# Kernel optimization log

Hardware: AMD Instinct MI355X
Metric: run time of the kernel (lower is better)

Reference implementation:

```python
import jax, jax.numpy as jnp
import numpy as np

B, A, M, C = 8, 100000, 32, 80
ALPHA, GAMMA = 0.25, 2.0
NORM = np.array([[0.1, 0.1, 0.2, 0.2]], dtype=np.float32)


def setup_inputs() -> dict:
    key = jax.random.key(0)
    k1, k2, k3, k4, k5, k6, k7, k8 = jax.random.split(key, 8)
    classifications = jax.random.uniform(k1, (B, A, C), dtype=jnp.float32)
    reggressions = jax.random.normal(k2, (B, A, 4), dtype=jnp.float32)
    # valid anchors: positive width/height boxes inside a ~640px image
    ctr = jax.random.uniform(k3, (1, A, 2), dtype=jnp.float32) * 600.0 + 20.0
    wh = jax.random.uniform(k4, (1, A, 2), dtype=jnp.float32) * 96.0 + 16.0
    anchors = jnp.concatenate([ctr - 0.5 * wh, ctr + 0.5 * wh], axis=-1)
    # annotations: [x1,y1,x2,y2,class], class=-1 marks padding
    xy1 = jax.random.uniform(k5, (B, M, 2), dtype=jnp.float32) * 500.0
    gwh = jax.random.uniform(k6, (B, M, 2), dtype=jnp.float32) * 112.0 + 8.0
    cls = jax.random.randint(k7, (B, M), 0, C).astype(jnp.float32)
    pad = jax.random.uniform(k8, (B, M)) < 0.3
    cls = jnp.where(pad, -1.0, cls)
    annotations = jnp.concatenate([xy1, xy1 + gwh, cls[..., None]], axis=-1)
    return {"classifications": classifications, "reggressions": reggressions,
            "anchors": anchors, "annotations": annotations}


def _calc_iou(a, b):
    # a: [A,4], b: [M,4] -> [A,M]
    area = (b[:, 2] - b[:, 0]) * (b[:, 3] - b[:, 1])
    iw = jnp.minimum(a[:, 2, None], b[None, :, 2]) - jnp.maximum(a[:, 0, None], b[None, :, 0])
    ih = jnp.minimum(a[:, 3, None], b[None, :, 3]) - jnp.maximum(a[:, 1, None], b[None, :, 1])
    iw = jnp.clip(iw, 0.0)
    ih = jnp.clip(ih, 0.0)
    ua = ((a[:, 2] - a[:, 0]) * (a[:, 3] - a[:, 1]))[:, None] + area[None, :] - iw * ih
    ua = jnp.clip(ua, 1e-8)
    return iw * ih / ua


def _focal_loss(classifications, reggressions, anchors, annotations):
    anchor = anchors[0]  # [A,4]
    aw = anchor[:, 2] - anchor[:, 0]
    ah = anchor[:, 3] - anchor[:, 1]
    acx = anchor[:, 0] + 0.5 * aw
    acy = anchor[:, 1] + 0.5 * ah
    norm = jnp.asarray(NORM)

    def per_image(cls_p, reg_p, annot):
        valid = annot[:, 4] != -1.0  # [M]
        has_valid = valid.any()
        cls_p = jnp.clip(cls_p, 1e-4, 1.0 - 1e-4)
        iou = _calc_iou(anchor, annot[:, :4])            # [A,M]
        iou = jnp.where(valid[None, :], iou, -1.0)       # mask padded annots
        iou_max = iou.max(axis=1)                        # [A]
        iou_arg = iou.argmax(axis=1)                     # [A]
        assigned = annot[iou_arg]                        # [A,5]
        pos = iou_max >= 0.5
        neg = iou_max < 0.4
        onehot = jax.nn.one_hot(assigned[:, 4].astype(jnp.int32), cls_p.shape[-1], dtype=cls_p.dtype)
        targets = jnp.where(pos[:, None], onehot,
                            jnp.where(neg[:, None], 0.0, -1.0))  # [A,C]
        alpha_f = jnp.where(targets == 1.0, ALPHA, 1.0 - ALPHA)
        focal_w = jnp.where(targets == 1.0, 1.0 - cls_p, cls_p)
        focal_w = alpha_f * focal_w ** GAMMA
        bce = -(targets * jnp.log(cls_p) + (1.0 - targets) * jnp.log(1.0 - cls_p))
        cls_loss = jnp.where(targets != -1.0, focal_w * bce, 0.0)
        num_pos = pos.sum().astype(cls_p.dtype)
        cls_total = jnp.where(has_valid,
                              cls_loss.sum() / jnp.maximum(num_pos, 1.0), 0.0)
        gw = jnp.clip(assigned[:, 2] - assigned[:, 0], 0.0)
        gh = jnp.clip(assigned[:, 3] - assigned[:, 1], 0.0)
        gcx = assigned[:, 0] + 0.5 * (assigned[:, 2] - assigned[:, 0])
        gcy = assigned[:, 1] + 0.5 * (assigned[:, 3] - assigned[:, 1])
        dx = (gcx - acx) / aw
        dy = (gcy - acy) / ah
        dw = jnp.log(jnp.where(pos, gw, aw) / aw)  # safe log on non-positives
        dh = jnp.log(jnp.where(pos, gh, ah) / ah)
        t = jnp.stack([dx, dy, dw, dh], axis=1) / norm  # [A,4]
        diff = jnp.abs(t - reg_p)
        rl = jnp.where(diff <= 1.0 / 9.0, 0.5 * 9.0 * diff ** 2, diff - 5.0 / 9.0)
        reg_total = jnp.where(num_pos > 0,
                              (rl * pos[:, None]).sum() / (4.0 * jnp.maximum(num_pos, 1.0)),
                              0.0)
        return cls_total, reg_total

    cls_l, reg_l = jax.vmap(per_image)(classifications, reggressions, annotations)
    return cls_l.mean().reshape(1), reg_l.mean().reshape(1)


def reference(classifications, reggressions, anchors, annotations):
    return _focal_loss(classifications, reggressions, anchors, annotations)
```

## Files before the change

kernel.cpp:

```cpp
#include <hip/hip_runtime.h>
#include <cstdint>
#include <cstddef>

#define NB 8
#define NA 100000
#define NM 32
#define NC 80
#define BLK 256
#define NBLK ((NA + BLK - 1) / BLK)
#define LN2F 0.69314718056f


__global__ __launch_bounds__(256) void fused_kernel(
    const float* __restrict__ cls,
    const float* __restrict__ regs,
    const float* __restrict__ anchors,
    const float* __restrict__ annots,
    float4* __restrict__ parts)
{
    const int b   = blockIdx.y;
    const int blk = blockIdx.x;
    const int tid = threadIdx.x;
    const int a   = blk * BLK + tid;

    __shared__ float sann[NM * 5];
    __shared__ float sw[BLK];
    __shared__ float sred[4 * 3];

    if (tid < NM * 5) sann[tid] = annots[b * NM * 5 + tid];
    __syncthreads();

    float reg_acc = 0.f;
    float posf    = 0.f;
    float corr    = 0.f;
    int   st      = 201;

    if (a < NA) {
        const float4 av = reinterpret_cast<const float4*>(anchors)[a];
        const float ax1 = av.x, ay1 = av.y, ax2 = av.z, ay2 = av.w;
        const float aw = ax2 - ax1, ah = ay2 - ay1;
        const float aarea = aw * ah;

        float best = -1e30f;
        int   barg = 0;
        #pragma unroll
        for (int m = 0; m < NM; ++m) {
            const float bx1 = sann[m * 5 + 0];
            const float by1 = sann[m * 5 + 1];
            const float bx2 = sann[m * 5 + 2];
            const float by2 = sann[m * 5 + 3];
            const float bc  = sann[m * 5 + 4];
            const float area = (bx2 - bx1) * (by2 - by1);
            float iw = fminf(ax2, bx2) - fmaxf(ax1, bx1);
            float ih = fminf(ay2, by2) - fmaxf(ay1, by1);
            iw = fmaxf(iw, 0.f);
            ih = fmaxf(ih, 0.f);
            const float inter = iw * ih;
            const float ua = fmaxf(aarea + area - inter, 1e-8f);
            float iou = inter * __builtin_amdgcn_rcpf(ua);
            if (bc == -1.0f) iou = -1.0f;
            if (iou > best) { best = iou; barg = m; }
        }

        if (best >= 0.5f) {
            const float bx1 = sann[barg * 5 + 0];
            const float by1 = sann[barg * 5 + 1];
            const float bx2 = sann[barg * 5 + 2];
            const float by2 = sann[barg * 5 + 3];
            st   = (int)sann[barg * 5 + 4];
            posf = 1.f;
            const float gw  = fmaxf(bx2 - bx1, 0.f);
            const float gh  = fmaxf(by2 - by1, 0.f);
            const float gcx = bx1 + 0.5f * (bx2 - bx1);
            const float gcy = by1 + 0.5f * (by2 - by1);
            const float acx = ax1 + 0.5f * aw;
            const float acy = ay1 + 0.5f * ah;
            const float t0 = ((gcx - acx) / aw) * 10.f;
            const float t1 = ((gcy - acy) / ah) * 10.f;
            const float t2 = __logf(gw / aw) * 5.f;
            const float t3 = __logf(gh / ah) * 5.f;
            const float4 rp = reinterpret_cast<const float4*>(regs)[(size_t)b * NA + a];
            const float d0 = fabsf(t0 - rp.x);
            const float d1 = fabsf(t1 - rp.y);
            const float d2 = fabsf(t2 - rp.z);
            const float d3 = fabsf(t3 - rp.w);
            const float TH = 1.f / 9.f;
            const float C59 = 5.f / 9.f;
            reg_acc  = (d0 <= TH) ? 4.5f * d0 * d0 : d0 - C59;
            reg_acc += (d1 <= TH) ? 4.5f * d1 * d1 : d1 - C59;
            reg_acc += (d2 <= TH) ? 4.5f * d2 * d2 : d2 - C59;
            reg_acc += (d3 <= TH) ? 4.5f * d3 * d3 : d3 - C59;
            const float pr  = cls[((size_t)b * NA + a) * NC + st];
            const float pt  = __builtin_amdgcn_fmed3f(pr, 1e-4f, 0.9999f);
            const float omt = 1.f - pt;
            corr = -0.25f * omt * omt * __logf(pt) + 0.75f * (pt * pt) * __logf(omt);
        } else if (best < 0.4f) {
            st = 200;
        }
    }
    sw[tid] = (st == 201) ? 0.f : 0.75f;
    __syncthreads();

    const int na_blk = min(BLK, NA - blk * BLK);
    const int n4 = na_blk * (NC / 4);
    const float4* __restrict__ p4 =
        reinterpret_cast<const float4*>(cls) + ((size_t)b * NA + (size_t)blk * BLK) * (NC / 4);

    float sneg = 0.f;
    int al  = tid / 20;
    int rem = tid - al * 20;
    #pragma unroll 5
    for (int k = 0; k < BLK * (NC / 4) / BLK; ++k) {
        const int i   = k * BLK + tid;
        const int ild = min(i, n4 - 1);
        const float4 v = p4[ild];
        const float wgt = (i < n4) ? sw[al] : 0.f;
        float g = 0.f;
        {
            const float p0 = __builtin_amdgcn_fmed3f(v.x, 1e-4f, 0.9999f);
            g = __fmaf_rn(p0 * p0, __log2f(1.f - p0), g);
            const float p1 = __builtin_amdgcn_fmed3f(v.y, 1e-4f, 0.9999f);
            g = __fmaf_rn(p1 * p1, __log2f(1.f - p1), g);
            const float p2 = __builtin_amdgcn_fmed3f(v.z, 1e-4f, 0.9999f);
            g = __fmaf_rn(p2 * p2, __log2f(1.f - p2), g);
            const float p3 = __builtin_amdgcn_fmed3f(v.w, 1e-4f, 0.9999f);
            g = __fmaf_rn(p3 * p3, __log2f(1.f - p3), g);
        }
        sneg = __fmaf_rn(wgt, g, sneg);
        rem += 16;
        const int c = (rem >= 20) ? 1 : 0;
        al  += 12 + c;
        rem -= c * 20;
    }

    float cacc = __fmaf_rn(-LN2F, sneg, corr);

    float r = reg_acc;
    float p = posf;
    #pragma unroll
    for (int off = 32; off; off >>= 1) {
        cacc += __shfl_down(cacc, off);
        r    += __shfl_down(r, off);
        p    += __shfl_down(p, off);
    }
    const int w = tid >> 6;
    if ((tid & 63) == 0) {
        sred[w * 3 + 0] = cacc;
        sred[w * 3 + 1] = r;
        sred[w * 3 + 2] = p;
    }
    __syncthreads();
    if (tid == 0) {
        float C = 0.f, R = 0.f, P = 0.f;
        #pragma unroll
        for (int i = 0; i < 4; ++i) {
            C += sred[i * 3 + 0];
            R += sred[i * 3 + 1];
            P += sred[i * 3 + 2];
        }
        parts[b * NBLK + blk] = make_float4(C, R, P, 0.f);
    }
}

__global__ __launch_bounds__(512) void finalize_kernel(
    const float* __restrict__ annots,
    const float4* __restrict__ parts,
    float* __restrict__ out)
{
    const int tid  = threadIdx.x;
    const int b    = tid >> 6;
    const int lane = tid & 63;
    __shared__ float simg[NB * 2];

    float C = 0.f, R = 0.f, P = 0.f;
    for (int i = lane; i < NBLK; i += 64) {
        const float4 v = parts[b * NBLK + i];
        C += v.x; R += v.y; P += v.z;
    }
    #pragma unroll
    for (int off = 32; off; off >>= 1) {
        C += __shfl_down(C, off);
        R += __shfl_down(R, off);
        P += __shfl_down(P, off);
    }
    const bool vld = (lane < NM) && (annots[b * NM * 5 + lane * 5 + 4] != -1.0f);
    const unsigned long long m = __ballot(vld);
    if (lane == 0) {
        const bool hv = (m != 0ULL);
        const float d = fmaxf(P, 1.f);
        simg[b * 2 + 0] = hv ? C / d : 0.f;
        simg[b * 2 + 1] = (P > 0.f) ? R / (4.f * d) : 0.f;
    }
    __syncthreads();
    if (tid == 0) {
        float cm = 0.f, rm = 0.f;
        #pragma unroll
        for (int i = 0; i < NB; ++i) {
            cm += simg[i * 2 + 0];
            rm += simg[i * 2 + 1];
        }
        out[0] = cm * (1.f / NB);
        out[1] = rm * (1.f / NB);
    }
}

extern "C" void kernel_launch(void* const* d_in, const int* in_sizes, int n_in,
                              void* d_out, int out_size, void* d_ws, size_t ws_size,
                              hipStream_t stream) {
    const float* cls     = (const float*)d_in[0];
    const float* regs    = (const float*)d_in[1];
    const float* anchors = (const float*)d_in[2];
    const float* annots  = (const float*)d_in[3];
    float* out = (float*)d_out;

    float4* parts = (float4*)d_ws;

    dim3 g1(NBLK, NB);
    fused_kernel<<<g1, BLK, 0, stream>>>(cls, regs, anchors, annots, parts);
    finalize_kernel<<<1, 512, 0, stream>>>(annots, parts, out);
}
```

Baseline: 50.30 us.

## Prefetch classification tiles before IoU phase and double-buffer the negative-loss stream

Block size grows from 256 to 512 threads, with the anchor-to-class index stepping constants and the reduction buffer resized to match. The first four float4 classification loads, plus the anchor load, are issued before the initial barrier so they overlap the IoU/argmax phase. The negative focal-loss loop is restructured into five groups of four loads, with the next group prefetched while the current one is computed. This aims to hide global memory latency in a bandwidth-bound stream, at the cost of more registers per thread and fewer blocks per CU.

```diff
diff --git a/kernel.cpp b/kernel.cpp
--- a/kernel.cpp
+++ b/kernel.cpp
@@ -6,12 +6,27 @@
 #define NA 100000
 #define NM 32
 #define NC 80
-#define BLK 256
+#define BLK 512
 #define NBLK ((NA + BLK - 1) / BLK)
 #define LN2F 0.69314718056f
 
-
-__global__ __launch_bounds__(256) void fused_kernel(
+#define ALQ 25
+#define ALR 12
+
+
+__device__ __forceinline__ float neg_term(const float4 v) {
+    const float p0 = __builtin_amdgcn_fmed3f(v.x, 1e-4f, 0.9999f);
+    float g = p0 * p0 * __log2f(1.f - p0);
+    const float p1 = __builtin_amdgcn_fmed3f(v.y, 1e-4f, 0.9999f);
+    g = __fmaf_rn(p1 * p1, __log2f(1.f - p1), g);
+    const float p2 = __builtin_amdgcn_fmed3f(v.z, 1e-4f, 0.9999f);
+    g = __fmaf_rn(p2 * p2, __log2f(1.f - p2), g);
+    const float p3 = __builtin_amdgcn_fmed3f(v.w, 1e-4f, 0.9999f);
+    g = __fmaf_rn(p3 * p3, __log2f(1.f - p3), g);
+    return g;
+}
+
+__global__ __launch_bounds__(512) void fused_kernel(
     const float* __restrict__ cls,
     const float* __restrict__ regs,
     const float* __restrict__ anchors,
@@ -25,9 +40,23 @@
 
     __shared__ float sann[NM * 5];
     __shared__ float sw[BLK];
-    __shared__ float sred[4 * 3];
+    __shared__ float sred[8 * 3];
 
     if (tid < NM * 5) sann[tid] = annots[b * NM * 5 + tid];
+
+    const float4 av = reinterpret_cast<const float4*>(anchors)[min(a, NA - 1)];
+
+    const int na_blk = min(BLK, NA - blk * BLK);
+    const int n4     = na_blk * (NC / 4);
+    const int n4m1   = n4 - 1;
+    const float4* __restrict__ p4 =
+        reinterpret_cast<const float4*>(cls) + ((size_t)b * NA + (size_t)blk * BLK) * (NC / 4);
+
+    float4 v0 = p4[min(0 * BLK + tid, n4m1)];
+    float4 v1 = p4[min(1 * BLK + tid, n4m1)];
+    float4 v2 = p4[min(2 * BLK + tid, n4m1)];
+    float4 v3 = p4[min(3 * BLK + tid, n4m1)];
+
     __syncthreads();
 
     float reg_acc = 0.f;
@@ -36,7 +65,6 @@
     int   st      = 201;
 
     if (a < NA) {
-        const float4 av = reinterpret_cast<const float4*>(anchors)[a];
         const float ax1 = av.x, ay1 = av.y, ax2 = av.z, ay2 = av.w;
         const float aw = ax2 - ax1, ah = ay2 - ay1;
         const float aarea = aw * ah;
@@ -101,36 +129,34 @@
     sw[tid] = (st == 201) ? 0.f : 0.75f;
     __syncthreads();
 
-    const int na_blk = min(BLK, NA - blk * BLK);
-    const int n4 = na_blk * (NC / 4);
-    const float4* __restrict__ p4 =
-        reinterpret_cast<const float4*>(cls) + ((size_t)b * NA + (size_t)blk * BLK) * (NC / 4);
-
     float sneg = 0.f;
     int al  = tid / 20;
     int rem = tid - al * 20;
-    #pragma unroll 5
-    for (int k = 0; k < BLK * (NC / 4) / BLK; ++k) {
-        const int i   = k * BLK + tid;
-        const int ild = min(i, n4 - 1);
-        const float4 v = p4[ild];
-        const float wgt = (i < n4) ? sw[al] : 0.f;
-        float g = 0.f;
-        {
-            const float p0 = __builtin_amdgcn_fmed3f(v.x, 1e-4f, 0.9999f);
-            g = __fmaf_rn(p0 * p0, __log2f(1.f - p0), g);
-            const float p1 = __builtin_amdgcn_fmed3f(v.y, 1e-4f, 0.9999f);
-            g = __fmaf_rn(p1 * p1, __log2f(1.f - p1), g);
-            const float p2 = __builtin_amdgcn_fmed3f(v.z, 1e-4f, 0.9999f);
-            g = __fmaf_rn(p2 * p2, __log2f(1.f - p2), g);
-            const float p3 = __builtin_amdgcn_fmed3f(v.w, 1e-4f, 0.9999f);
-            g = __fmaf_rn(p3 * p3, __log2f(1.f - p3), g);
-        }
-        sneg = __fmaf_rn(wgt, g, sneg);
-        rem += 16;
-        const int c = (rem >= 20) ? 1 : 0;
-        al  += 12 + c;
-        rem -= c * 20;
+
+    #pragma unroll
+    for (int kk = 0; kk < 5; ++kk) {
+        const float4 c0 = v0, c1 = v1, c2 = v2, c3 = v3;
+        if (kk < 4) {
+            const int nb4 = (kk * 4 + 4) * BLK + tid;
+            v0 = p4[min(nb4 + 0 * BLK, n4m1)];
+            v1 = p4[min(nb4 + 1 * BLK, n4m1)];
+            v2 = p4[min(nb4 + 2 * BLK, n4m1)];
+            v3 = p4[min(nb4 + 3 * BLK, n4m1)];
+        }
+        const int i0 = kk * 4 * BLK + tid;
+        float w[4];
+        #pragma unroll
+        for (int q = 0; q < 4; ++q) {
+            w[q] = (i0 + q * BLK <= n4m1) ? sw[al] : 0.f;
+            rem += ALR;
+            const int c = (rem >= 20) ? 1 : 0;
+            al  += ALQ + c;
+            rem -= c * 20;
+        }
+        sneg = __fmaf_rn(w[0], neg_term(c0), sneg);
+        sneg = __fmaf_rn(w[1], neg_term(c1), sneg);
+        sneg = __fmaf_rn(w[2], neg_term(c2), sneg);
+        sneg = __fmaf_rn(w[3], neg_term(c3), sneg);
     }
 
     float cacc = __fmaf_rn(-LN2F, sneg, corr);
@@ -153,7 +179,7 @@
     if (tid == 0) {
         float C = 0.f, R = 0.f, P = 0.f;
         #pragma unroll
-        for (int i = 0; i < 4; ++i) {
+        for (int i = 0; i < 8; ++i) {
             C += sred[i * 3 + 0];
             R += sred[i * 3 + 1];
             P += sred[i * 3 + 2];
```

Measured after the change: 53.22 us. 5.8% more time.
